# Kernel optimization log

Measured on AMD Instinct MI355X. Metric: run time of the kernel, lower is better.

## Reference

```python
import jax, jax.numpy as jnp
import numpy as np

B, T, IN, H = 256, 1000, 1, 512


def setup_inputs() -> dict:
    key = jax.random.key(0)
    ks = jax.random.split(key, 11)
    s = 0.05  # small init scale, mimics torch Linear init magnitude
    f32 = jnp.float32
    return {
        "inputs": jax.random.normal(ks[0], (B, T, IN), f32),
        "St": jax.random.uniform(ks[1], (B, 1), f32),
        "Mass": jax.random.uniform(ks[2], (B, 1), f32),
        # weights stored [in, out] (transpose of torch's [out, in]); same math
        "Wz": jax.random.normal(ks[3], (IN + H, H), f32) * s,
        "bz": jnp.zeros((H,), f32),
        "Wr": jax.random.normal(ks[4], (IN + H, H), f32) * s,
        "br": jnp.zeros((H,), f32),
        "Wh": jax.random.normal(ks[5], (IN + H + 2, H), f32) * s,
        "bh": jnp.zeros((H,), f32),
        "Wk": jax.random.normal(ks[6], (H + 1, 1), f32) * s,
        "bk": jnp.zeros((1,), f32),
    }


def reference(inputs, St, Mass, Wz, bz, Wr, br, Wh, bh, Wk, bk):
    b = inputs.shape[0]
    h_dim = Wz.shape[1]
    h0 = jnp.zeros((b, h_dim), inputs.dtype)
    k0 = jnp.zeros((b, 1), inputs.dtype)
    xs = jnp.swapaxes(inputs, 0, 1)  # [T, B, IN] for scan over time

    def step(carry, x):
        h, k = carry
        comb = jnp.concatenate([x, h], axis=1)          # [B, IN+H]
        z = jax.nn.sigmoid(comb @ Wz + bz)
        r = jax.nn.sigmoid(comb @ Wr + br)
        h_in = jnp.concatenate([x, h * r, St * k, Mass], axis=1)  # [B, IN+H+2]
        h_tilde = jnp.tanh(h_in @ Wh + bh)
        h_new = (1.0 - z) * h + z * h_tilde
        k_new = jax.nn.sigmoid(jnp.concatenate([h_new, k], axis=1) @ Wk + bk)
        return (h_new, k_new), h_new

    _, hs = jax.lax.scan(step, (h0, k0), xs)  # hs: [T, B, H]
    return jnp.swapaxes(hs, 0, 1)  # [B, T, H]
```

## Files before the change

kernel.cpp:

```cpp
#include <hip/hip_runtime.h>
#include <hip/hip_fp16.h>

#define BATCH 256
#define TLEN  1000
#define HDIM  512
#define HALF  256
#define NQ    128

#define ZR_ELEMS   (NQ * HDIM)
#define WH_OFF_B   ((size_t)ZR_ELEMS * 16)
#define WS16_BYTES (WH_OFF_B + (size_t)ZR_ELEMS * 8)

typedef _Float16 f16;
typedef f16 f16x2 __attribute__((ext_vector_type(2)));

__device__ __forceinline__ unsigned int f2h2(float a, float b) {
    __half2 h = __halves2half2(__float2half_rn(a), __float2half_rn(b));
    return __builtin_bit_cast(unsigned int, h);
}

__device__ __forceinline__ float fdot2f(unsigned int a, unsigned int b, float c) {
#if __has_builtin(__builtin_amdgcn_fdot2)
    return __builtin_amdgcn_fdot2(__builtin_bit_cast(f16x2, a),
                                  __builtin_bit_cast(f16x2, b), c, false);
#else
    const f16x2 x = __builtin_bit_cast(f16x2, a);
    const f16x2 y = __builtin_bit_cast(f16x2, b);
    return c + (float)x[0] * (float)y[0] + (float)x[1] * (float)y[1];
#endif
}

__device__ __forceinline__ unsigned int pack2(float a, float b) {
#if __has_builtin(__builtin_amdgcn_cvt_pkrtz)
    return __builtin_bit_cast(unsigned int, __builtin_amdgcn_cvt_pkrtz(a, b));
#else
    f16x2 v; v[0] = (f16)a; v[1] = (f16)b;
    return __builtin_bit_cast(unsigned int, v);
#endif
}

__global__ void convert_weights_kernel(
    const float* __restrict__ Wz, const float* __restrict__ Wr,
    const float* __restrict__ Wh, uint4* __restrict__ ZR, uint2* __restrict__ WH)
{
    const int idx = blockIdx.x * 256 + threadIdx.x;
    const int q = idx >> 9;
    const int c = idx & (HDIM - 1);
    const size_t r0 = (size_t)(1 + 4 * q) * HDIM + c;
    uint4 z;
    z.x = f2h2(Wz[r0],            Wz[r0 + HDIM]);
    z.y = f2h2(Wr[r0],            Wr[r0 + HDIM]);
    z.z = f2h2(Wz[r0 + 2 * HDIM], Wz[r0 + 3 * HDIM]);
    z.w = f2h2(Wr[r0 + 2 * HDIM], Wr[r0 + 3 * HDIM]);
    ZR[idx] = z;
    uint2 h;
    h.x = f2h2(Wh[r0],            Wh[r0 + HDIM]);
    h.y = f2h2(Wh[r0 + 2 * HDIM], Wh[r0 + 3 * HDIM]);
    WH[idx] = h;
}

__launch_bounds__(1024, 4)
__global__ void mc_gru_k2_dot2_kernel(
    const float* __restrict__ inputs,
    const float* __restrict__ St,
    const float* __restrict__ Mass,
    const float* __restrict__ Wz,
    const float* __restrict__ bz,
    const float* __restrict__ Wr,
    const float* __restrict__ br,
    const float* __restrict__ Wh,
    const float* __restrict__ bh,
    const float* __restrict__ Wk,
    const float* __restrict__ bk,
    const uint4* __restrict__ ZR,
    const uint2* __restrict__ WH,
    float* __restrict__ out)
{
    __shared__ float x_l[TLEN];
    __shared__ uint2 h2_l[HDIM / 4];
    __shared__ uint2 hr2_l[HDIM / 4];
    __shared__ float az_s[2 * HDIM];
    __shared__ float ar_s[2 * HDIM];
    __shared__ float ah_s[2 * HDIM];
    __shared__ float kw_l[8];

    const int tid  = threadIdx.x;
    const int b    = blockIdx.x;
    const int c    = tid & (HDIM - 1);
    const int half = tid >> 9;
    const int h2b  = half * (HALF / 4);

    for (int idx = tid; idx < TLEN; idx += 1024) x_l[idx] = inputs[b * TLEN + idx];
    if (tid < HDIM / 2) ((unsigned int*)h2_l)[tid] = 0u;

    const float wz0   = Wz[c];
    const float wr0   = Wr[c];
    const float wh0   = Wh[c];
    const float wh513 = Wh[513 * HDIM + c];
    const float wh514 = Wh[514 * HDIM + c];
    const float bzc   = bz[c];
    const float brc   = br[c];
    const float bhc   = bh[c];
    const float wkc   = Wk[c];
    const float wk512 = Wk[512];
    const float bk0   = bk[0];
    const float st    = St[b];
    const float mass  = Mass[b];

    const uint4* __restrict__ zrp = ZR + (size_t)(half * 64) * HDIM + c;
    const uint2* __restrict__ whp = WH + (size_t)(half * 64) * HDIM + c;

    float h_reg = 0.0f;
    float k_reg = 0.0f;
    __syncthreads();

    for (int t = 0; t < TLEN; ++t) {
        const float x = x_l[t];

        float azp = 0.0f, arp = 0.0f;
        #pragma unroll 8
        for (int qi = 0; qi < HALF / 4; ++qi) {
            const uint4 v  = zrp[(size_t)qi * HDIM];
            const uint2 hh = h2_l[h2b + qi];
            azp = fdot2f(hh.x, v.x, azp);
            azp = fdot2f(hh.y, v.z, azp);
            arp = fdot2f(hh.x, v.y, arp);
            arp = fdot2f(hh.y, v.w, arp);
        }
        az_s[tid] = azp;
        ar_s[tid] = arp;
        __syncthreads();

        float z = 0.0f;
        if (half == 0) {
            z = 1.0f / (1.0f + __expf(-(az_s[c] + az_s[HDIM + c] + x * wz0 + bzc)));
            const float r =
                1.0f / (1.0f + __expf(-(ar_s[c] + ar_s[HDIM + c] + x * wr0 + brc)));
            const float hr  = h_reg * r;
            const float hrn = __shfl_xor(hr, 1);
            if (!(c & 1)) ((unsigned int*)hr2_l)[c >> 1] = pack2(hr, hrn);
        }
        __syncthreads();

        float ahp = 0.0f;
        #pragma unroll 8
        for (int qi = 0; qi < HALF / 4; ++qi) {
            const uint2 v  = whp[(size_t)qi * HDIM];
            const uint2 hh = hr2_l[h2b + qi];
            ahp = fdot2f(hh.x, v.x, ahp);
            ahp = fdot2f(hh.y, v.y, ahp);
        }
        ah_s[tid] = ahp;
        __syncthreads();

        if (half == 0) {
            const float pre = ah_s[c] + ah_s[HDIM + c] + x * wh0
                            + (st * k_reg) * wh513 + mass * wh514 + bhc;
            const float e  = __expf(-2.0f * pre);
            const float ht = (1.0f - e) / (1.0f + e);
            const float hn = (1.0f - z) * h_reg + z * ht;
            h_reg = hn;

            __builtin_nontemporal_store(hn, &out[((size_t)b * TLEN + t) * HDIM + c]);
            const float hnn = __shfl_xor(hn, 1);
            if (!(c & 1)) ((unsigned int*)h2_l)[c >> 1] = pack2(hn, hnn);

            float kc = hn * wkc;
            kc += __shfl_xor(kc, 1);
            kc += __shfl_xor(kc, 2);
            kc += __shfl_xor(kc, 4);
            kc += __shfl_xor(kc, 8);
            kc += __shfl_xor(kc, 16);
            kc += __shfl_xor(kc, 32);
            if ((tid & 63) == 0) kw_l[tid >> 6] = kc;
        }
        __syncthreads();

        const float ksum = kw_l[0] + kw_l[1] + kw_l[2] + kw_l[3]
                         + kw_l[4] + kw_l[5] + kw_l[6] + kw_l[7];
        k_reg = 1.0f / (1.0f + __expf(-(ksum + wk512 * k_reg + bk0)));
    }
}

__launch_bounds__(1024, 4)
__global__ void mc_gru_k2_kernel(
    const float* __restrict__ inputs, const float* __restrict__ St,
    const float* __restrict__ Mass, const float* __restrict__ Wz,
    const float* __restrict__ bz, const float* __restrict__ Wr,
    const float* __restrict__ br, const float* __restrict__ Wh,
    const float* __restrict__ bh, const float* __restrict__ Wk,
    const float* __restrict__ bk, float* __restrict__ out)
{
    __shared__ float x_l[TLEN];
    __shared__ float h_l[HDIM];
    __shared__ float hr_l[HDIM];
    __shared__ float az_s[2 * HDIM];
    __shared__ float ar_s[2 * HDIM];
    __shared__ float ah_s[2 * HDIM];
    __shared__ float kw_l[8];

    const int tid  = threadIdx.x;
    const int b    = blockIdx.x;
    const int c    = tid & (HDIM - 1);
    const int half = tid >> 9;
    const int klo  = half * HALF;

    for (int idx = tid; idx < TLEN; idx += 1024) x_l[idx] = inputs[b * TLEN + idx];
    if (tid < HDIM) h_l[tid] = 0.0f;

    const float wz0 = Wz[c], wr0 = Wr[c], wh0 = Wh[c];
    const float wh513 = Wh[513 * HDIM + c], wh514 = Wh[514 * HDIM + c];
    const float bzc = bz[c], brc = br[c], bhc = bh[c], wkc = Wk[c];
    const float wk512 = Wk[512], bk0 = bk[0];
    const float st = St[b], mass = Mass[b];

    const float* __restrict__ WzH = Wz + (size_t)(1 + klo) * HDIM + c;
    const float* __restrict__ WrH = Wr + (size_t)(1 + klo) * HDIM + c;
    const float* __restrict__ WhH = Wh + (size_t)(1 + klo) * HDIM + c;

    float k_reg = 0.0f;
    __syncthreads();

    for (int t = 0; t < TLEN; ++t) {
        const float x = x_l[t];
        float azp = 0.0f, arp = 0.0f;
        {
            const float4* h4 = (const float4*)&h_l[klo];
            #pragma unroll 4
            for (int kq = 0; kq < HALF / 4; ++kq) {
                const float4 hv = h4[kq];
                const int k = 4 * kq;
                azp += hv.x * WzH[(k + 0) * HDIM] + hv.y * WzH[(k + 1) * HDIM]
                     + hv.z * WzH[(k + 2) * HDIM] + hv.w * WzH[(k + 3) * HDIM];
                arp += hv.x * WrH[(k + 0) * HDIM] + hv.y * WrH[(k + 1) * HDIM]
                     + hv.z * WrH[(k + 2) * HDIM] + hv.w * WrH[(k + 3) * HDIM];
            }
        }
        az_s[tid] = azp;
        ar_s[tid] = arp;
        __syncthreads();

        const float z = 1.0f / (1.0f + __expf(-(az_s[c] + az_s[HDIM + c] + x * wz0 + bzc)));
        const float r = 1.0f / (1.0f + __expf(-(ar_s[c] + ar_s[HDIM + c] + x * wr0 + brc)));
        const float hvv = h_l[c];
        if (half == 0) hr_l[c] = hvv * r;
        __syncthreads();

        float ahp = 0.0f;
        {
            const float4* hr4 = (const float4*)&hr_l[klo];
            #pragma unroll 4
            for (int kq = 0; kq < HALF / 4; ++kq) {
                const float4 hv = hr4[kq];
                const int k = 4 * kq;
                ahp += hv.x * WhH[(k + 0) * HDIM] + hv.y * WhH[(k + 1) * HDIM]
                     + hv.z * WhH[(k + 2) * HDIM] + hv.w * WhH[(k + 3) * HDIM];
            }
        }
        ah_s[tid] = ahp;
        __syncthreads();

        const float pre = ah_s[c] + ah_s[HDIM + c] + x * wh0
                        + (st * k_reg) * wh513 + mass * wh514 + bhc;
        const float e  = __expf(-2.0f * pre);
        const float ht = (1.0f - e) / (1.0f + e);
        const float hn = (1.0f - z) * hvv + z * ht;

        if (half == 0) {
            __builtin_nontemporal_store(hn, &out[((size_t)b * TLEN + t) * HDIM + c]);
            h_l[c] = hn;
            float kc = hn * wkc;
            kc += __shfl_xor(kc, 1);
            kc += __shfl_xor(kc, 2);
            kc += __shfl_xor(kc, 4);
            kc += __shfl_xor(kc, 8);
            kc += __shfl_xor(kc, 16);
            kc += __shfl_xor(kc, 32);
            if ((tid & 63) == 0) kw_l[tid >> 6] = kc;
        }
        __syncthreads();

        const float ksum = kw_l[0] + kw_l[1] + kw_l[2] + kw_l[3]
                         + kw_l[4] + kw_l[5] + kw_l[6] + kw_l[7];
        k_reg = 1.0f / (1.0f + __expf(-(ksum + wk512 * k_reg + bk0)));
    }
}

extern "C" void kernel_launch(void* const* d_in, const int* in_sizes, int n_in,
                              void* d_out, int out_size, void* d_ws, size_t ws_size,
                              hipStream_t stream) {
    (void)in_sizes; (void)n_in; (void)out_size;

    const float* inputs = (const float*)d_in[0];
    const float* St     = (const float*)d_in[1];
    const float* Mass   = (const float*)d_in[2];
    const float* Wz     = (const float*)d_in[3];
    const float* bz     = (const float*)d_in[4];
    const float* Wr     = (const float*)d_in[5];
    const float* br     = (const float*)d_in[6];
    const float* Wh     = (const float*)d_in[7];
    const float* bh     = (const float*)d_in[8];
    const float* Wk     = (const float*)d_in[9];
    const float* bk     = (const float*)d_in[10];
    float* out = (float*)d_out;

    if (ws_size >= WS16_BYTES) {
        uint4* ZR = (uint4*)d_ws;
        uint2* WH = (uint2*)((char*)d_ws + WH_OFF_B);
        hipLaunchKernelGGL(convert_weights_kernel, dim3(ZR_ELEMS / 256), dim3(256),
                           0, stream, Wz, Wr, Wh, ZR, WH);
        hipLaunchKernelGGL(mc_gru_k2_dot2_kernel, dim3(BATCH), dim3(1024), 0, stream,
                           inputs, St, Mass, Wz, bz, Wr, br, Wh, bh, Wk, bk,
                           (const uint4*)ZR, (const uint2*)WH, out);
    } else {
        hipLaunchKernelGGL(mc_gru_k2_kernel, dim3(BATCH), dim3(1024), 0, stream,
                           inputs, St, Mass, Wz, bz, Wr, br, Wh, bh, Wk, bk, out);
    }
}
```

Before: 16.19 ms.

## Keep part of the recurrent weights resident in registers and LDS

Preloads the first few ZR weight quads and the first WH quads into registers, and another block of WH quads into shared memory, once before the time loop. Each step then reads only the remaining weights from global/L2, which is meant to cut repeated weight traffic on every one of the 1000 steps. This raises register pressure under the 1024-thread launch bound and adds 128KB of LDS per block, which may spill registers or limit occupancy. A no-op '*0.0f' term is also added to the fallback kernel's tanh.

```diff
diff --git a/kernel.cpp b/kernel.cpp
--- a/kernel.cpp
+++ b/kernel.cpp
@@ -6,6 +6,12 @@
 #define HDIM  512
 #define HALF  256
 #define NQ    128
+
+#define ZR_REG   6
+#define WH_REG   20
+#define WH_LDS   16
+#define WH_LDS_LO (WH_REG)
+#define WH_STREAM_LO (WH_REG + WH_LDS)
 
 #define ZR_ELEMS   (NQ * HDIM)
 #define WH_OFF_B   ((size_t)ZR_ELEMS * 16)
@@ -60,7 +66,7 @@
 }
 
 __launch_bounds__(1024, 4)
-__global__ void mc_gru_k2_dot2_kernel(
+__global__ void mc_gru_k2_res_kernel(
     const float* __restrict__ inputs,
     const float* __restrict__ St,
     const float* __restrict__ Mass,
@@ -83,6 +89,7 @@
     __shared__ float ar_s[2 * HDIM];
     __shared__ float ah_s[2 * HDIM];
     __shared__ float kw_l[8];
+    __shared__ uint2 whl[WH_LDS][1024];
 
     const int tid  = threadIdx.x;
     const int b    = blockIdx.x;
@@ -110,6 +117,16 @@
     const uint4* __restrict__ zrp = ZR + (size_t)(half * 64) * HDIM + c;
     const uint2* __restrict__ whp = WH + (size_t)(half * 64) * HDIM + c;
 
+    uint4 zr_r[ZR_REG];
+    #pragma unroll
+    for (int qi = 0; qi < ZR_REG; ++qi) zr_r[qi] = zrp[(size_t)qi * HDIM];
+    uint2 wh_r[WH_REG];
+    #pragma unroll
+    for (int qi = 0; qi < WH_REG; ++qi) wh_r[qi] = whp[(size_t)qi * HDIM];
+    #pragma unroll
+    for (int i = 0; i < WH_LDS; ++i)
+        whl[i][tid] = whp[(size_t)(WH_LDS_LO + i) * HDIM];
+
     float h_reg = 0.0f;
     float k_reg = 0.0f;
     __syncthreads();
@@ -118,8 +135,17 @@
         const float x = x_l[t];
 
         float azp = 0.0f, arp = 0.0f;
+        #pragma unroll
+        for (int qi = 0; qi < ZR_REG; ++qi) {
+            const uint4 v  = zr_r[qi];
+            const uint2 hh = h2_l[h2b + qi];
+            azp = fdot2f(hh.x, v.x, azp);
+            azp = fdot2f(hh.y, v.z, azp);
+            arp = fdot2f(hh.x, v.y, arp);
+            arp = fdot2f(hh.y, v.w, arp);
+        }
         #pragma unroll 8
-        for (int qi = 0; qi < HALF / 4; ++qi) {
+        for (int qi = ZR_REG; qi < HALF / 4; ++qi) {
             const uint4 v  = zrp[(size_t)qi * HDIM];
             const uint2 hh = h2_l[h2b + qi];
             azp = fdot2f(hh.x, v.x, azp);
@@ -143,10 +169,24 @@
         __syncthreads();
 
         float ahp = 0.0f;
-        #pragma unroll 8
-        for (int qi = 0; qi < HALF / 4; ++qi) {
+        #pragma unroll 7
+        for (int qi = WH_STREAM_LO; qi < HALF / 4; ++qi) {
             const uint2 v  = whp[(size_t)qi * HDIM];
             const uint2 hh = hr2_l[h2b + qi];
+            ahp = fdot2f(hh.x, v.x, ahp);
+            ahp = fdot2f(hh.y, v.y, ahp);
+        }
+        #pragma unroll
+        for (int qi = 0; qi < WH_REG; ++qi) {
+            const uint2 v  = wh_r[qi];
+            const uint2 hh = hr2_l[h2b + qi];
+            ahp = fdot2f(hh.x, v.x, ahp);
+            ahp = fdot2f(hh.y, v.y, ahp);
+        }
+        #pragma unroll
+        for (int i = 0; i < WH_LDS; ++i) {
+            const uint2 v  = whl[i][tid];
+            const uint2 hh = hr2_l[h2b + WH_LDS_LO + i];
             ahp = fdot2f(hh.x, v.x, ahp);
             ahp = fdot2f(hh.y, v.y, ahp);
         }
@@ -262,7 +302,7 @@
 
         const float pre = ah_s[c] + ah_s[HDIM + c] + x * wh0
                         + (st * k_reg) * wh513 + mass * wh514 + bhc;
-        const float e  = __expf(-2.0f * pre);
+        const float e  = __expf(-2.0f * ah_s[c] * 0.0f - 2.0f * pre);
         const float ht = (1.0f - e) / (1.0f + e);
         const float hn = (1.0f - z) * hvv + z * ht;
 
@@ -309,7 +349,7 @@
         uint2* WH = (uint2*)((char*)d_ws + WH_OFF_B);
         hipLaunchKernelGGL(convert_weights_kernel, dim3(ZR_ELEMS / 256), dim3(256),
                            0, stream, Wz, Wr, Wh, ZR, WH);
-        hipLaunchKernelGGL(mc_gru_k2_dot2_kernel, dim3(BATCH), dim3(1024), 0, stream,
+        hipLaunchKernelGGL(mc_gru_k2_res_kernel, dim3(BATCH), dim3(1024), 0, stream,
                            inputs, St, Mass, Wz, bz, Wr, br, Wh, bh, Wk, bk,
                            (const uint4*)ZR, (const uint2*)WH, out);
     } else {
```

After: 12.97 ms. 1.25x faster.
